# Kernel tuning notes

Measured on AMD Instinct MI355X. Metric: run time of the kernel, lower is better.

Reference implementation:

```python
import jax, jax.numpy as jnp
from jax import lax
import numpy as np

B, L, H, V = 256, 2048, 128, 32000
THR = 0.4      # energy_threshold
LN_EPS = 1e-5  # torch LayerNorm default


def setup_inputs() -> dict:
    key = jax.random.key(0)
    ks = jax.random.split(key, 12)
    s = lambda k, shp, scale: (jax.random.normal(k, shp, dtype=jnp.float32) * scale)
    return {
        "seq": jax.random.randint(ks[0], (B, L), 0, V),
        "embed": s(ks[1], (V, H), 0.02),
        "W1": s(ks[2], (H, 2 * H), H ** -0.5),
        "b1": jnp.zeros((2 * H,), jnp.float32),
        "W2": s(ks[3], (2 * H, H), (2 * H) ** -0.5),
        "b2": jnp.zeros((H,), jnp.float32),
        "gamma": jnp.ones((H,), jnp.float32),
        "beta": jnp.zeros((H,), jnp.float32),
        "Wrp": s(ks[4], (H, H), H ** -0.5),
        "brp": jnp.zeros((H,), jnp.float32),
        "Wout": s(ks[5], (H, V), H ** -0.5),
        "bout": jnp.zeros((V,), jnp.float32),
    }


def _encode(seq, embed, W1, b1, W2, b2, gamma, beta):
    e = embed[seq]                                         # [B,L,H]
    ff = jnp.maximum(e @ W1 + b1, 0.0) @ W2 + b2           # [B,L,H]
    y = e + ff
    mu = y.mean(-1, keepdims=True)
    var = ((y - mu) ** 2).mean(-1, keepdims=True)
    return (y - mu) * lax.rsqrt(var + LN_EPS) * gamma + beta


def reference(seq, embed, W1, b1, W2, b2, gamma, beta, Wrp, brp, Wout, bout):
    h_all = _encode(seq, embed, W1, b1, W2, b2, gamma, beta)  # [B,L,H]

    def step(M, k):
        # k = v = h_all[:, t, :]  -> [B,H]
        v = k
        vp = jnp.einsum('bij,bj->bi', M, k)
        error = v - vp / (jnp.sum(k * k, axis=-1, keepdims=True) + 1e-6)
        gate = (jnp.linalg.norm(error, axis=-1)
                > THR * jnp.linalg.norm(v, axis=-1)).astype(M.dtype)  # [B]
        M = M + gate[:, None, None] * jnp.einsum('bi,bj->bij', error, k)
        return M, None

    M0 = jnp.zeros((B, H, H), h_all.dtype)
    ks = jnp.swapaxes(h_all[:, :-1, :], 0, 1)               # [L-1,B,H]
    M_fin, _ = lax.scan(step, M0, ks)
    r = jnp.einsum('bij,bj->bi', M_fin, h_all[:, -1, :])    # [B,H]
    return (r @ Wrp + brp) @ Wout + bout                    # [B,V]
```

## Files before the change

### kernel.cpp

```cpp
#include <hip/hip_runtime.h>
#include <hip/hip_bf16.h>


#define BB 256
#define LL 2048
#define HH 128
#define VV 32000
#define RS 136

typedef float f32x2 __attribute__((ext_vector_type(2)));

__device__ __forceinline__ void dma16(const float* g, float* l) {
  __builtin_amdgcn_global_load_lds(
      (const __attribute__((address_space(1))) void*)g,
      (__attribute__((address_space(3))) void*)l,
      16, 0, 0);
}

template <int CTRL>
__device__ __forceinline__ float dppadd(float x) {
  int y = __builtin_amdgcn_update_dpp(0, __float_as_int(x), CTRL, 0xF, 0xF, true);
  return x + __int_as_float(y);
}

__device__ __forceinline__ void pkfma(f32x2& d, f32x2 a, f32x2 b) {
  asm("v_pk_fma_f32 %0, %1, %2, %0" : "+v"(d) : "v"(a), "v"(b));
}

__device__ __forceinline__ void barrier_lgkm() {
  asm volatile("s_waitcnt lgkmcnt(0)\n\ts_barrier" ::: "memory");
}
__device__ __forceinline__ void wait_vmN(int n) {
  if (n == 3)      asm volatile("s_waitcnt vmcnt(3)" ::: "memory");
  else if (n == 2) asm volatile("s_waitcnt vmcnt(2)" ::: "memory");
  else if (n == 1) asm volatile("s_waitcnt vmcnt(1)" ::: "memory");
  else             asm volatile("s_waitcnt vmcnt(0)" ::: "memory");
}

__global__ __launch_bounds__(256, 1) void build_htab_kernel(
    const float* __restrict__ embed,
    const float* __restrict__ W1,
    const float* __restrict__ b1,
    const float* __restrict__ W2,
    const float* __restrict__ b2,
    const float* __restrict__ gamma,
    const float* __restrict__ beta,
    float* __restrict__ Htab2)
{
  const int tid = threadIdx.x;
  const int j   = tid & 127;
  const int h2  = tid >> 7;

  float w1r[128];
#pragma unroll
  for (int m = 0; m < 128; ++m) w1r[m] = W1[m * 256 + tid];

  const float b1n = b1[tid];
  const float b2j = b2[j];
  const float gj  = gamma[j];
  const float bj  = beta[j];

  __shared__ __align__(16) float4 w2q[64][128];
  __shared__ __align__(16) float e_s[128];
  __shared__ __align__(16) float a_s[256];
  __shared__ float p_s[2][128];
  __shared__ float red[8];

  for (int idx = tid; idx < 8192; idx += 256) {
    int n4 = idx >> 7, jj = idx & 127;
    float4 w;
    w.x = W2[(size_t)(4 * n4 + 0) * 128 + jj];
    w.y = W2[(size_t)(4 * n4 + 1) * 128 + jj];
    w.z = W2[(size_t)(4 * n4 + 2) * 128 + jj];
    w.w = W2[(size_t)(4 * n4 + 3) * 128 + jj];
    w2q[n4][jj] = w;
  }
  __syncthreads();

  for (int v = blockIdx.x; v < VV; v += gridDim.x) {
    if (tid < 128) e_s[tid] = embed[(size_t)v * 128 + tid];
    __syncthreads();

    float acc[4] = {b1n, 0.f, 0.f, 0.f};
#pragma unroll
    for (int q = 0; q < 32; ++q) {
      float4 ev = *(const float4*)&e_s[4 * q];
      float t = ev.x * w1r[4 * q + 0];
      t = fmaf(ev.y, w1r[4 * q + 1], t);
      t = fmaf(ev.z, w1r[4 * q + 2], t);
      t = fmaf(ev.w, w1r[4 * q + 3], t);
      acc[q & 3] += t;
    }
    float a = fmaxf((acc[0] + acc[1]) + (acc[2] + acc[3]), 0.0f);
    a_s[tid] = a;
    __syncthreads();

    float p0 = 0.f, p1 = 0.f, p2v = 0.f, p3 = 0.f;
#pragma unroll
    for (int q = 0; q < 32; ++q) {
      int n4 = h2 * 32 + q;
      float4 av = *(const float4*)&a_s[4 * n4];
      float4 wq = w2q[n4][j];
      p0 = fmaf(av.x, wq.x, p0);
      p1 = fmaf(av.y, wq.y, p1);
      p2v = fmaf(av.z, wq.z, p2v);
      p3 = fmaf(av.w, wq.w, p3);
    }
    p_s[h2][j] = (p0 + p1) + (p2v + p3);
    __syncthreads();

    float y = 0.0f;
    if (tid < 128) {
      float ff = p_s[0][tid] + p_s[1][tid] + b2j;
      y = e_s[tid] + ff;
    }
    float s1 = y, s2 = y * y;
    s1 = dppadd<0xB1>(s1);  s2 = dppadd<0xB1>(s2);
    s1 = dppadd<0x4E>(s1);  s2 = dppadd<0x4E>(s2);
    s1 = dppadd<0x141>(s1); s2 = dppadd<0x141>(s2);
    s1 = dppadd<0x140>(s1); s2 = dppadd<0x140>(s2);
    s1 = dppadd<0x142>(s1); s2 = dppadd<0x142>(s2);
    s1 = dppadd<0x143>(s1); s2 = dppadd<0x143>(s2);
    if (tid < 128 && (tid & 63) == 63) {
      red[tid >> 6] = s1;
      red[2 + (tid >> 6)] = s2;
    }
    __syncthreads();
    float mu = (red[0] + red[1]) * (1.0f / 128.0f);
    float ms = (red[2] + red[3]) * (1.0f / 128.0f);
    float var = ms - mu * mu;
    float hv = 0.0f;
    if (tid < 128) {
      float dy = y - mu;
      hv = dy * (1.0f / sqrtf(var + 1e-5f)) * gj + bj;
      int ofs = tid + ((tid >> 6) << 2);
      Htab2[(size_t)v * RS + ofs] = hv;
    }
    float q2 = hv * hv;
    q2 = dppadd<0xB1>(q2);
    q2 = dppadd<0x4E>(q2);
    q2 = dppadd<0x141>(q2);
    q2 = dppadd<0x140>(q2);
    q2 = dppadd<0x142>(q2);
    q2 = dppadd<0x143>(q2);
    if (tid < 128 && (tid & 63) == 63) red[4 + (tid >> 6)] = q2;
    __syncthreads();
    if (tid == 0) {
      float kk = red[4] + red[5];
      Htab2[(size_t)v * RS + 132] = kk;
      Htab2[(size_t)v * RS + 133] = 1.0f / (kk + 1e-6f);
    }
    __syncthreads();
  }
}

__global__ __launch_bounds__(512, 1) void scan_kernel(
    const int* __restrict__ seq,
    const float* __restrict__ Htab2,
    const float* __restrict__ Wrp,
    const float* __restrict__ brp,
    float* __restrict__ rr)
{
  const int b     = blockIdx.x;
  const int tid   = threadIdx.x;
  const int lane  = tid & 63;
  const int wv    = tid >> 6;
  const int rg    = lane >> 4;
  const int cg    = lane & 15;
  const int i0    = wv * 16 + rg * 4;
  const int iofs  = i0 + ((i0 >> 6) << 2);
  const int kbase = (cg & 7) * 8 + (cg >> 3) * 68;

  __shared__ int seq_s[LL];
  __shared__ __align__(16) float slots[8][RS];
  __shared__ __align__(16) float red_s[4][8];
  __shared__ __align__(16) float r_s[128];
  __shared__ float p2_s[4][128];

  {
    int t0 = seq[(size_t)b * LL + 0];
    int t1 = seq[(size_t)b * LL + 1];
    int t2 = seq[(size_t)b * LL + 2];
    int t3 = seq[(size_t)b * LL + 3];
    if (lane < 34) {
      dma16(Htab2 + (size_t)t0 * RS + lane * 4, &slots[0][0]);
      dma16(Htab2 + (size_t)t1 * RS + lane * 4, &slots[1][0]);
      dma16(Htab2 + (size_t)t2 * RS + lane * 4, &slots[2][0]);
      dma16(Htab2 + (size_t)t3 * RS + lane * 4, &slots[3][0]);
    }
  }
  for (int t = tid; t < LL; t += 512) seq_s[t] = seq[(size_t)b * LL + t];
  __syncthreads();

  f32x2 M00{0.f,0.f}, M01{0.f,0.f}, M02{0.f,0.f}, M03{0.f,0.f};
  f32x2 M10{0.f,0.f}, M11{0.f,0.f}, M12{0.f,0.f}, M13{0.f,0.f};
  f32x2 M20{0.f,0.f}, M21{0.f,0.f}, M22{0.f,0.f}, M23{0.f,0.f};
  f32x2 M30{0.f,0.f}, M31{0.f,0.f}, M32{0.f,0.f}, M33{0.f,0.f};

  f32x2 kA0, kA1, kA2, kA3, kB0, kB1, kB2, kB3;
  float4 kiA, kiB;
  float kkA, invA, kkB, invB;
  {
    const f32x2* kp = (const f32x2*)&slots[0][kbase];
    kA0 = kp[0]; kA1 = kp[1]; kA2 = kp[2]; kA3 = kp[3];
    kiA = *(const float4*)&slots[0][iofs];
    float2 kv = *(const float2*)&slots[0][132];
    kkA = kv.x; invA = kv.y;
    asm volatile("" : "+v"(kA0), "+v"(kA1), "+v"(kA2), "+v"(kA3));
    asm volatile("" : "+v"(kiA.x), "+v"(kiA.y), "+v"(kiA.z), "+v"(kiA.w));
    asm volatile("" : "+v"(kkA), "+v"(invA));
  }

  auto step = [&](f32x2& kc0, f32x2& kc1, f32x2& kc2, f32x2& kc3,
                  float4& kic, float kk_c, float inv_c,
                  f32x2& kn0, f32x2& kn1, f32x2& kn2, f32x2& kn3,
                  float4& kin, float& kk_n, float& inv_n,
                  int t, int p, int sn, int sd, int nwait) {
    if (nwait == 3) {
      int tk = seq_s[t + 4];
      if (lane < 34)
        dma16(Htab2 + (size_t)tk * RS + lane * 4, &slots[sd][0]);
    }
    f32x2 a0{0.f,0.f}, a1{0.f,0.f}, a2{0.f,0.f}, a3{0.f,0.f};
    pkfma(a0, kc0, M00); pkfma(a0, kc1, M01); pkfma(a0, kc2, M02); pkfma(a0, kc3, M03);
    pkfma(a1, kc0, M10); pkfma(a1, kc1, M11); pkfma(a1, kc2, M12); pkfma(a1, kc3, M13);
    pkfma(a2, kc0, M20); pkfma(a2, kc1, M21); pkfma(a2, kc2, M22); pkfma(a2, kc3, M23);
    pkfma(a3, kc0, M30); pkfma(a3, kc1, M31); pkfma(a3, kc2, M32); pkfma(a3, kc3, M33);
    float v0 = a0.x + a0.y, v1 = a1.x + a1.y;
    float v2 = a2.x + a2.y, v3 = a3.x + a3.y;
    v0 = dppadd<0xB1>(v0);  v1 = dppadd<0xB1>(v1);
    v2 = dppadd<0xB1>(v2);  v3 = dppadd<0xB1>(v3);
    v0 = dppadd<0x4E>(v0);  v1 = dppadd<0x4E>(v1);
    v2 = dppadd<0x4E>(v2);  v3 = dppadd<0x4E>(v3);
    v0 = dppadd<0x141>(v0); v1 = dppadd<0x141>(v1);
    v2 = dppadd<0x141>(v2); v3 = dppadd<0x141>(v3);
    v0 = dppadd<0x140>(v0); v1 = dppadd<0x140>(v1);
    v2 = dppadd<0x140>(v2); v3 = dppadd<0x140>(v3);
    float e0 = fmaf(-v0, inv_c, kic.x);
    float e1 = fmaf(-v1, inv_c, kic.y);
    float e2 = fmaf(-v2, inv_c, kic.z);
    float e3 = fmaf(-v3, inv_c, kic.w);
    float s = fmaf(e3, e3, fmaf(e2, e2, fmaf(e1, e1, e0 * e0)));
    s = dppadd<0x142>(s);
    s = dppadd<0x143>(s);
    if (lane == 63) red_s[p][wv] = s;
    barrier_lgkm();

    float4 ra = *(const float4*)&red_s[p][0];
    float4 rb = *(const float4*)&red_s[p][4];
    wait_vmN(nwait);
    {
      const f32x2* kp = (const f32x2*)&slots[sn][kbase];
      kn0 = kp[0]; kn1 = kp[1]; kn2 = kp[2]; kn3 = kp[3];
      kin = *(const float4*)&slots[sn][iofs];
      float2 kv = *(const float2*)&slots[sn][132];
      kk_n = kv.x; inv_n = kv.y;
    }
    float ne2 = ((ra.x + ra.y) + (ra.z + ra.w)) + ((rb.x + rb.y) + (rb.z + rb.w));
    int g = ne2 > 0.16f * kk_c;
    float ge0 = g ? e0 : 0.0f;
    float ge1 = g ? e1 : 0.0f;
    float ge2 = g ? e2 : 0.0f;
    float ge3 = g ? e3 : 0.0f;
    f32x2 g0{ge0, ge0}, g1{ge1, ge1}, g2{ge2, ge2}, g3{ge3, ge3};
    pkfma(M00, g0, kc0); pkfma(M01, g0, kc1); pkfma(M02, g0, kc2); pkfma(M03, g0, kc3);
    pkfma(M10, g1, kc0); pkfma(M11, g1, kc1); pkfma(M12, g1, kc2); pkfma(M13, g1, kc3);
    pkfma(M20, g2, kc0); pkfma(M21, g2, kc1); pkfma(M22, g2, kc2); pkfma(M23, g2, kc3);
    pkfma(M30, g3, kc0); pkfma(M31, g3, kc1); pkfma(M32, g3, kc2); pkfma(M33, g3, kc3);
    asm volatile("" : "+v"(kn0), "+v"(kn1), "+v"(kn2), "+v"(kn3));
    asm volatile("" : "+v"(kin.x), "+v"(kin.y), "+v"(kin.z), "+v"(kin.w));
    asm volatile("" : "+v"(kk_n), "+v"(inv_n));
  };

  for (int t = 0; t < 2040; t += 8) {
    step(kA0,kA1,kA2,kA3, kiA, kkA, invA, kB0,kB1,kB2,kB3, kiB, kkB, invB, t + 0, 0, 1, 4, 3);
    step(kB0,kB1,kB2,kB3, kiB, kkB, invB, kA0,kA1,kA2,kA3, kiA, kkA, invA, t + 1, 1, 2, 5, 3);
    step(kA0,kA1,kA2,kA3, kiA, kkA, invA, kB0,kB1,kB2,kB3, kiB, kkB, invB, t + 2, 2, 3, 6, 3);
    step(kB0,kB1,kB2,kB3, kiB, kkB, invB, kA0,kA1,kA2,kA3, kiA, kkA, invA, t + 3, 3, 4, 7, 3);
    step(kA0,kA1,kA2,kA3, kiA, kkA, invA, kB0,kB1,kB2,kB3, kiB, kkB, invB, t + 4, 0, 5, 0, 3);
    step(kB0,kB1,kB2,kB3, kiB, kkB, invB, kA0,kA1,kA2,kA3, kiA, kkA, invA, t + 5, 1, 6, 1, 3);
    step(kA0,kA1,kA2,kA3, kiA, kkA, invA, kB0,kB1,kB2,kB3, kiB, kkB, invB, t + 6, 2, 7, 2, 3);
    step(kB0,kB1,kB2,kB3, kiB, kkB, invB, kA0,kA1,kA2,kA3, kiA, kkA, invA, t + 7, 3, 0, 3, 3);
  }
  step(kA0,kA1,kA2,kA3, kiA, kkA, invA, kB0,kB1,kB2,kB3, kiB, kkB, invB, 2040, 0, 1, 4, 3);
  step(kB0,kB1,kB2,kB3, kiB, kkB, invB, kA0,kA1,kA2,kA3, kiA, kkA, invA, 2041, 1, 2, 5, 3);
  step(kA0,kA1,kA2,kA3, kiA, kkA, invA, kB0,kB1,kB2,kB3, kiB, kkB, invB, 2042, 2, 3, 6, 3);
  step(kB0,kB1,kB2,kB3, kiB, kkB, invB, kA0,kA1,kA2,kA3, kiA, kkA, invA, 2043, 3, 4, 7, 3);
  step(kA0,kA1,kA2,kA3, kiA, kkA, invA, kB0,kB1,kB2,kB3, kiB, kkB, invB, 2044, 0, 5, 0, 2);
  step(kB0,kB1,kB2,kB3, kiB, kkB, invB, kA0,kA1,kA2,kA3, kiA, kkA, invA, 2045, 1, 6, 1, 1);
  step(kA0,kA1,kA2,kA3, kiA, kkA, invA, kB0,kB1,kB2,kB3, kiB, kkB, invB, 2046, 2, 7, 2, 0);

  {
    f32x2 a0{0.f,0.f}, a1{0.f,0.f}, a2{0.f,0.f}, a3{0.f,0.f};
    pkfma(a0, kB0, M00); pkfma(a0, kB1, M01); pkfma(a0, kB2, M02); pkfma(a0, kB3, M03);
    pkfma(a1, kB0, M10); pkfma(a1, kB1, M11); pkfma(a1, kB2, M12); pkfma(a1, kB3, M13);
    pkfma(a2, kB0, M20); pkfma(a2, kB1, M21); pkfma(a2, kB2, M22); pkfma(a2, kB3, M23);
    pkfma(a3, kB0, M30); pkfma(a3, kB1, M31); pkfma(a3, kB2, M32); pkfma(a3, kB3, M33);
    float v0 = a0.x + a0.y, v1 = a1.x + a1.y;
    float v2 = a2.x + a2.y, v3 = a3.x + a3.y;
    v0 = dppadd<0xB1>(v0);  v1 = dppadd<0xB1>(v1);
    v2 = dppadd<0xB1>(v2);  v3 = dppadd<0xB1>(v3);
    v0 = dppadd<0x4E>(v0);  v1 = dppadd<0x4E>(v1);
    v2 = dppadd<0x4E>(v2);  v3 = dppadd<0x4E>(v3);
    v0 = dppadd<0x141>(v0); v1 = dppadd<0x141>(v1);
    v2 = dppadd<0x141>(v2); v3 = dppadd<0x141>(v3);
    v0 = dppadd<0x140>(v0); v1 = dppadd<0x140>(v1);
    v2 = dppadd<0x140>(v2); v3 = dppadd<0x140>(v3);
    if (cg == 0) {
      *(float4*)&r_s[i0] = float4{v0, v1, v2, v3};
    }
  }
  __syncthreads();

  const int j = tid & 127;
  const int g = tid >> 7;
  float pac[2] = {0.f, 0.f};
#pragma unroll
  for (int m = 0; m < 32; ++m) {
    pac[m & 1] = fmaf(r_s[g * 32 + m],
                      Wrp[(size_t)(g * 32 + m) * 128 + j], pac[m & 1]);
  }
  p2_s[g][j] = pac[0] + pac[1];
  __syncthreads();
  if (tid < 128) {
    rr[(size_t)b * 128 + tid] =
        p2_s[0][tid] + p2_s[1][tid] + p2_s[2][tid] + p2_s[3][tid] + brp[tid];
  }
}

__global__ __launch_bounds__(256, 1) void out_kernel(
    const float* __restrict__ rr,
    const float* __restrict__ Wout,
    const float* __restrict__ bout,
    float* __restrict__ out)
{
  const int tid = threadIdx.x;
  const int v = blockIdx.x * 64 + (tid & 63);
  const int bg = tid >> 6;
  const int b0 = blockIdx.y * 64;

  __shared__ float4 rs4[64][32];
  for (int idx = tid; idx < 2048; idx += 256) {
    int bb = idx >> 5, q = idx & 31;
    rs4[bb][q] = ((const float4*)rr)[(size_t)(b0 + bb) * 32 + q];
  }
  __syncthreads();

  float acc[16];
#pragma unroll
  for (int m = 0; m < 16; ++m) acc[m] = 0.0f;

  for (int h4 = 0; h4 < 32; ++h4) {
    float w0 = Wout[(size_t)(4 * h4 + 0) * VV + v];
    float w1 = Wout[(size_t)(4 * h4 + 1) * VV + v];
    float w2 = Wout[(size_t)(4 * h4 + 2) * VV + v];
    float w3 = Wout[(size_t)(4 * h4 + 3) * VV + v];
#pragma unroll
    for (int m = 0; m < 16; ++m) {
      float4 rv = rs4[bg * 16 + m][h4];
      float t = rv.x * w0;
      t = fmaf(rv.y, w1, t);
      t = fmaf(rv.z, w2, t);
      t = fmaf(rv.w, w3, t);
      acc[m] += t;
    }
  }
  float bo = bout[v];
#pragma unroll
  for (int m = 0; m < 16; ++m) {
    out[(size_t)(b0 + bg * 16 + m) * VV + v] = acc[m] + bo;
  }
}

extern "C" void kernel_launch(void* const* d_in, const int* in_sizes, int n_in,
                              void* d_out, int out_size, void* d_ws, size_t ws_size,
                              hipStream_t stream)
{
  const int* seq      = (const int*)d_in[0];
  const float* embed  = (const float*)d_in[1];
  const float* W1     = (const float*)d_in[2];
  const float* b1     = (const float*)d_in[3];
  const float* W2     = (const float*)d_in[4];
  const float* b2     = (const float*)d_in[5];
  const float* gamma  = (const float*)d_in[6];
  const float* beta   = (const float*)d_in[7];
  const float* Wrp    = (const float*)d_in[8];
  const float* brp    = (const float*)d_in[9];
  const float* Wout   = (const float*)d_in[10];
  const float* bout   = (const float*)d_in[11];
  float* out          = (float*)d_out;

  char* ws = (char*)d_ws;
  float* Htab2 = (float*)ws;
  float* rr    = (float*)(ws + 17408000);

  hipLaunchKernelGGL(build_htab_kernel, dim3(256), dim3(256), 0, stream,
                     embed, W1, b1, W2, b2, gamma, beta, Htab2);
  hipLaunchKernelGGL(scan_kernel, dim3(BB), dim3(512), 0, stream,
                     seq, Htab2, Wrp, brp, rr);
  hipLaunchKernelGGL(out_kernel, dim3(VV / 64, 4), dim3(256), 0, stream,
                     rr, Wout, bout, out);
}
```

Baseline: 1.460 ms.

## Process two scan steps per barrier using rank-one correction algebra

Restructures the sequential delta-rule scan so each block handles two tokens per superstep. The second token's error and gate are derived algebraically from the first token's error (via e·a, e·e, k0·k1 dot products reduced together), so only one cross-wave barrier and reduction is needed per two steps. This halves the barrier and LDS reduction count on the serial critical path, at the cost of extra FMAs, more registers for two in-flight token sets, and reordered floating-point arithmetic that may differ slightly near the gate threshold.

```diff
diff --git a/kernel.cpp b/kernel.cpp
--- a/kernel.cpp
+++ b/kernel.cpp
@@ -31,8 +31,7 @@
   asm volatile("s_waitcnt lgkmcnt(0)\n\ts_barrier" ::: "memory");
 }
 __device__ __forceinline__ void wait_vmN(int n) {
-  if (n == 3)      asm volatile("s_waitcnt vmcnt(3)" ::: "memory");
-  else if (n == 2) asm volatile("s_waitcnt vmcnt(2)" ::: "memory");
+  if (n == 2)      asm volatile("s_waitcnt vmcnt(2)" ::: "memory");
   else if (n == 1) asm volatile("s_waitcnt vmcnt(1)" ::: "memory");
   else             asm volatile("s_waitcnt vmcnt(0)" ::: "memory");
 }
@@ -173,9 +172,16 @@
 
   __shared__ int seq_s[LL];
   __shared__ __align__(16) float slots[8][RS];
-  __shared__ __align__(16) float red_s[4][8];
+  __shared__ __align__(16) float4 red4[3][8];
+  __shared__ __align__(16) float red1[8];
   __shared__ __align__(16) float r_s[128];
   __shared__ float p2_s[4][128];
+
+  struct KTok {
+    f32x2 c0, c1, c2, c3;
+    float ki0, ki1, ki2, ki3;
+    float kk, inv;
+  };
 
   {
     int t0 = seq[(size_t)b * LL + 0];
@@ -197,37 +203,26 @@
   f32x2 M20{0.f,0.f}, M21{0.f,0.f}, M22{0.f,0.f}, M23{0.f,0.f};
   f32x2 M30{0.f,0.f}, M31{0.f,0.f}, M32{0.f,0.f}, M33{0.f,0.f};
 
-  f32x2 kA0, kA1, kA2, kA3, kB0, kB1, kB2, kB3;
-  float4 kiA, kiB;
-  float kkA, invA, kkB, invB;
-  {
-    const f32x2* kp = (const f32x2*)&slots[0][kbase];
-    kA0 = kp[0]; kA1 = kp[1]; kA2 = kp[2]; kA3 = kp[3];
-    kiA = *(const float4*)&slots[0][iofs];
-    float2 kv = *(const float2*)&slots[0][132];
-    kkA = kv.x; invA = kv.y;
-    asm volatile("" : "+v"(kA0), "+v"(kA1), "+v"(kA2), "+v"(kA3));
-    asm volatile("" : "+v"(kiA.x), "+v"(kiA.y), "+v"(kiA.z), "+v"(kiA.w));
-    asm volatile("" : "+v"(kkA), "+v"(invA));
-  }
-
-  auto step = [&](f32x2& kc0, f32x2& kc1, f32x2& kc2, f32x2& kc3,
-                  float4& kic, float kk_c, float inv_c,
-                  f32x2& kn0, f32x2& kn1, f32x2& kn2, f32x2& kn3,
-                  float4& kin, float& kk_n, float& inv_n,
-                  int t, int p, int sn, int sd, int nwait) {
-    if (nwait == 3) {
-      int tk = seq_s[t + 4];
-      if (lane < 34)
-        dma16(Htab2 + (size_t)tk * RS + lane * 4, &slots[sd][0]);
-    }
+  auto loadTok = [&](KTok& T, const float* sp) {
+    const f32x2* kp = (const f32x2*)(sp + kbase);
+    T.c0 = kp[0]; T.c1 = kp[1]; T.c2 = kp[2]; T.c3 = kp[3];
+    float4 k4 = *(const float4*)(sp + iofs);
+    T.ki0 = k4.x; T.ki1 = k4.y; T.ki2 = k4.z; T.ki3 = k4.w;
+    float2 kv = *(const float2*)(sp + 132);
+    T.kk = kv.x; T.inv = kv.y;
+  };
+  auto pinTok = [&](KTok& T) {
+    asm volatile("" : "+v"(T.c0), "+v"(T.c1), "+v"(T.c2), "+v"(T.c3));
+    asm volatile("" : "+v"(T.ki0), "+v"(T.ki1), "+v"(T.ki2), "+v"(T.ki3));
+    asm volatile("" : "+v"(T.kk), "+v"(T.inv));
+  };
+  auto rowdot = [&](const KTok& K, float& v0, float& v1, float& v2, float& v3) {
     f32x2 a0{0.f,0.f}, a1{0.f,0.f}, a2{0.f,0.f}, a3{0.f,0.f};
-    pkfma(a0, kc0, M00); pkfma(a0, kc1, M01); pkfma(a0, kc2, M02); pkfma(a0, kc3, M03);
-    pkfma(a1, kc0, M10); pkfma(a1, kc1, M11); pkfma(a1, kc2, M12); pkfma(a1, kc3, M13);
-    pkfma(a2, kc0, M20); pkfma(a2, kc1, M21); pkfma(a2, kc2, M22); pkfma(a2, kc3, M23);
-    pkfma(a3, kc0, M30); pkfma(a3, kc1, M31); pkfma(a3, kc2, M32); pkfma(a3, kc3, M33);
-    float v0 = a0.x + a0.y, v1 = a1.x + a1.y;
-    float v2 = a2.x + a2.y, v3 = a3.x + a3.y;
+    pkfma(a0, K.c0, M00); pkfma(a0, K.c1, M01); pkfma(a0, K.c2, M02); pkfma(a0, K.c3, M03);
+    pkfma(a1, K.c0, M10); pkfma(a1, K.c1, M11); pkfma(a1, K.c2, M12); pkfma(a1, K.c3, M13);
+    pkfma(a2, K.c0, M20); pkfma(a2, K.c1, M21); pkfma(a2, K.c2, M22); pkfma(a2, K.c3, M23);
+    pkfma(a3, K.c0, M30); pkfma(a3, K.c1, M31); pkfma(a3, K.c2, M32); pkfma(a3, K.c3, M33);
+    v0 = a0.x + a0.y; v1 = a1.x + a1.y; v2 = a2.x + a2.y; v3 = a3.x + a3.y;
     v0 = dppadd<0xB1>(v0);  v1 = dppadd<0xB1>(v1);
     v2 = dppadd<0xB1>(v2);  v3 = dppadd<0xB1>(v3);
     v0 = dppadd<0x4E>(v0);  v1 = dppadd<0x4E>(v1);
@@ -236,76 +231,125 @@
     v2 = dppadd<0x141>(v2); v3 = dppadd<0x141>(v3);
     v0 = dppadd<0x140>(v0); v1 = dppadd<0x140>(v1);
     v2 = dppadd<0x140>(v2); v3 = dppadd<0x140>(v3);
-    float e0 = fmaf(-v0, inv_c, kic.x);
-    float e1 = fmaf(-v1, inv_c, kic.y);
-    float e2 = fmaf(-v2, inv_c, kic.z);
-    float e3 = fmaf(-v3, inv_c, kic.w);
+  };
+
+  KTok P0{}, P1{}, Q0{}, Q1{};
+  loadTok(P0, &slots[0][0]);
+  loadTok(P1, &slots[1][0]);
+  pinTok(P0); pinTok(P1);
+
+  int p = 0;
+
+  auto superstep = [&](KTok& C0, KTok& C1, KTok& R0, KTok& R1,
+                       int t, int sr0, int sr1, int sd0, int sd1,
+                       int nwait, int doIssue) {
+    if (doIssue) {
+      int tk0 = seq_s[t + 4];
+      int tk1 = seq_s[t + 5];
+      if (lane < 34) {
+        dma16(Htab2 + (size_t)tk0 * RS + lane * 4, &slots[sd0][0]);
+        dma16(Htab2 + (size_t)tk1 * RS + lane * 4, &slots[sd1][0]);
+      }
+    }
+    float u0, u1, u2, u3, w0, w1, w2, w3;
+    rowdot(C0, u0, u1, u2, u3);
+    rowdot(C1, w0, w1, w2, w3);
+    float e0 = fmaf(-C0.inv, u0, C0.ki0);
+    float e1 = fmaf(-C0.inv, u1, C0.ki1);
+    float e2 = fmaf(-C0.inv, u2, C0.ki2);
+    float e3 = fmaf(-C0.inv, u3, C0.ki3);
+    float aa0 = fmaf(-C1.inv, w0, C1.ki0);
+    float aa1 = fmaf(-C1.inv, w1, C1.ki1);
+    float aa2 = fmaf(-C1.inv, w2, C1.ki2);
+    float aa3 = fmaf(-C1.inv, w3, C1.ki3);
+    float sE  = fmaf(e3, e3, fmaf(e2, e2, fmaf(e1, e1, e0 * e0)));
+    float sC  = fmaf(C0.ki3, C1.ki3, fmaf(C0.ki2, C1.ki2, fmaf(C0.ki1, C1.ki1, C0.ki0 * C1.ki0)));
+    float sAE = fmaf(aa3, e3, fmaf(aa2, e2, fmaf(aa1, e1, aa0 * e0)));
+    float sA  = fmaf(aa3, aa3, fmaf(aa2, aa2, fmaf(aa1, aa1, aa0 * aa0)));
+    sE = dppadd<0x142>(sE);  sC = dppadd<0x142>(sC);
+    sAE = dppadd<0x142>(sAE); sA = dppadd<0x142>(sA);
+    sE = dppadd<0x143>(sE);  sC = dppadd<0x143>(sC);
+    sAE = dppadd<0x143>(sAE); sA = dppadd<0x143>(sA);
+    if (lane == 63) red4[p][wv] = float4{sE, sC, sAE, sA};
+    barrier_lgkm();
+    const float4* rp = (const float4*)&red4[p][0];
+    float4 q0 = rp[0], q1 = rp[1], q2 = rp[2], q3 = rp[3];
+    float4 q4 = rp[4], q5 = rp[5], q6 = rp[6], q7 = rp[7];
+    wait_vmN(nwait);
+    loadTok(R0, &slots[sr0][0]);
+    loadTok(R1, &slots[sr1][0]);
+    float SE  = ((q0.x + q1.x) + (q2.x + q3.x)) + ((q4.x + q5.x) + (q6.x + q7.x));
+    float SC  = ((q0.y + q1.y) + (q2.y + q3.y)) + ((q4.y + q5.y) + (q6.y + q7.y));
+    float SAE = ((q0.z + q1.z) + (q2.z + q3.z)) + ((q4.z + q5.z) + (q6.z + q7.z));
+    float SA  = ((q0.w + q1.w) + (q2.w + q3.w)) + ((q4.w + q5.w) + (q6.w + q7.w));
+    int gA = SE > 0.16f * C0.kk;
+    float phi = gA ? (C1.inv * SC) : 0.0f;
+    float E1 = fmaf(phi, fmaf(phi, SE, -2.0f * SAE), SA);
+    int gB = E1 > 0.16f * C1.kk;
+    float f0 = gA ? e0 : 0.0f;
+    float f1 = gA ? e1 : 0.0f;
+    float f2 = gA ? e2 : 0.0f;
+    float f3 = gA ? e3 : 0.0f;
+    float h0 = fmaf(-phi, e0, aa0);
+    float h1 = fmaf(-phi, e1, aa1);
+    float h2 = fmaf(-phi, e2, aa2);
+    float h3 = fmaf(-phi, e3, aa3);
+    float j0 = gB ? h0 : 0.0f;
+    float j1 = gB ? h1 : 0.0f;
+    float j2 = gB ? h2 : 0.0f;
+    float j3 = gB ? h3 : 0.0f;
+    f32x2 F0{f0, f0}, F1{f1, f1}, F2{f2, f2}, F3{f3, f3};
+    f32x2 J0{j0, j0}, J1{j1, j1}, J2{j2, j2}, J3{j3, j3};
+    pkfma(M00, F0, C0.c0); pkfma(M01, F0, C0.c1); pkfma(M02, F0, C0.c2); pkfma(M03, F0, C0.c3);
+    pkfma(M10, F1, C0.c0); pkfma(M11, F1, C0.c1); pkfma(M12, F1, C0.c2); pkfma(M13, F1, C0.c3);
+    pkfma(M20, F2, C0.c0); pkfma(M21, F2, C0.c1); pkfma(M22, F2, C0.c2); pkfma(M23, F2, C0.c3);
+    pkfma(M30, F3, C0.c0); pkfma(M31, F3, C0.c1); pkfma(M32, F3, C0.c2); pkfma(M33, F3, C0.c3);
+    pkfma(M00, J0, C1.c0); pkfma(M01, J0, C1.c1); pkfma(M02, J0, C1.c2); pkfma(M03, J0, C1.c3);
+    pkfma(M10, J1, C1.c0); pkfma(M11, J1, C1.c1); pkfma(M12, J1, C1.c2); pkfma(M13, J1, C1.c3);
+    pkfma(M20, J2, C1.c0); pkfma(M21, J2, C1.c1); pkfma(M22, J2, C1.c2); pkfma(M23, J2, C1.c3);
+    pkfma(M30, J3, C1.c0); pkfma(M31, J3, C1.c1); pkfma(M32, J3, C1.c2); pkfma(M33, J3, C1.c3);
+    pinTok(R0); pinTok(R1);
+    p = (p == 2) ? 0 : (p + 1);
+  };
+
+  for (int it = 0; it < 255; ++it) {
+    int T = it * 8;
+    superstep(P0, P1, Q0, Q1, T + 0, 2, 3, 4, 5, 2, 1);
+    superstep(Q0, Q1, P0, P1, T + 2, 4, 5, 6, 7, 2, 1);
+    superstep(P0, P1, Q0, Q1, T + 4, 6, 7, 0, 1, 2, 1);
+    superstep(Q0, Q1, P0, P1, T + 6, 0, 1, 2, 3, 2, 1);
+  }
+  superstep(P0, P1, Q0, Q1, 2040, 2, 3, 4, 5, 2, 1);
+  superstep(Q0, Q1, P0, P1, 2042, 4, 5, 6, 7, 2, 1);
+  superstep(P0, P1, Q0, Q1, 2044, 6, 7, 0, 1, 0, 0);
+
+  {
+    float u0, u1, u2, u3;
+    rowdot(Q0, u0, u1, u2, u3);
+    float e0 = fmaf(-Q0.inv, u0, Q0.ki0);
+    float e1 = fmaf(-Q0.inv, u1, Q0.ki1);
+    float e2 = fmaf(-Q0.inv, u2, Q0.ki2);
+    float e3 = fmaf(-Q0.inv, u3, Q0.ki3);
     float s = fmaf(e3, e3, fmaf(e2, e2, fmaf(e1, e1, e0 * e0)));
     s = dppadd<0x142>(s);
     s = dppadd<0x143>(s);
-    if (lane == 63) red_s[p][wv] = s;
+    if (lane == 63) red1[wv] = s;
     barrier_lgkm();
-
-    float4 ra = *(const float4*)&red_s[p][0];
-    float4 rb = *(const float4*)&red_s[p][4];
-    wait_vmN(nwait);
-    {
-      const f32x2* kp = (const f32x2*)&slots[sn][kbase];
-      kn0 = kp[0]; kn1 = kp[1]; kn2 = kp[2]; kn3 = kp[3];
-      kin = *(const float4*)&slots[sn][iofs];
-      float2 kv = *(const float2*)&slots[sn][132];
-      kk_n = kv.x; inv_n = kv.y;
-    }
-    float ne2 = ((ra.x + ra.y) + (ra.z + ra.w)) + ((rb.x + rb.y) + (rb.z + rb.w));
-    int g = ne2 > 0.16f * kk_c;
-    float ge0 = g ? e0 : 0.0f;
-    float ge1 = g ? e1 : 0.0f;
-    float ge2 = g ? e2 : 0.0f;
-    float ge3 = g ? e3 : 0.0f;
-    f32x2 g0{ge0, ge0}, g1{ge1, ge1}, g2{ge2, ge2}, g3{ge3, ge3};
-    pkfma(M00, g0, kc0); pkfma(M01, g0, kc1); pkfma(M02, g0, kc2); pkfma(M03, g0, kc3);
-    pkfma(M10, g1, kc0); pkfma(M11, g1, kc1); pkfma(M12, g1, kc2); pkfma(M13, g1, kc3);
-    pkfma(M20, g2, kc0); pkfma(M21, g2, kc1); pkfma(M22, g2, kc2); pkfma(M23, g2, kc3);
-    pkfma(M30, g3, kc0); pkfma(M31, g3, kc1); pkfma(M32, g3, kc2); pkfma(M33, g3, kc3);
-    asm volatile("" : "+v"(kn0), "+v"(kn1), "+v"(kn2), "+v"(kn3));
-    asm volatile("" : "+v"(kin.x), "+v"(kin.y), "+v"(kin.z), "+v"(kin.w));
-    asm volatile("" : "+v"(kk_n), "+v"(inv_n));
-  };
-
-  for (int t = 0; t < 2040; t += 8) {
-    step(kA0,kA1,kA2,kA3, kiA, kkA, invA, kB0,kB1,kB2,kB3, kiB, kkB, invB, t + 0, 0, 1, 4, 3);
-    step(kB0,kB1,kB2,kB3, kiB, kkB, invB, kA0,kA1,kA2,kA3, kiA, kkA, invA, t + 1, 1, 2, 5, 3);
-    step(kA0,kA1,kA2,kA3, kiA, kkA, invA, kB0,kB1,kB2,kB3, kiB, kkB, invB, t + 2, 2, 3, 6, 3);
-    step(kB0,kB1,kB2,kB3, kiB, kkB, invB, kA0,kA1,kA2,kA3, kiA, kkA, invA, t + 3, 3, 4, 7, 3);
-    step(kA0,kA1,kA2,kA3, kiA, kkA, invA, kB0,kB1,kB2,kB3, kiB, kkB, invB, t + 4, 0, 5, 0, 3);
-    step(kB0,kB1,kB2,kB3, kiB, kkB, invB, kA0,kA1,kA2,kA3, kiA, kkA, invA, t + 5, 1, 6, 1, 3);
-    step(kA0,kA1,kA2,kA3, kiA, kkA, invA, kB0,kB1,kB2,kB3, kiB, kkB, invB, t + 6, 2, 7, 2, 3);
-    step(kB0,kB1,kB2,kB3, kiB, kkB, invB, kA0,kA1,kA2,kA3, kiA, kkA, invA, t + 7, 3, 0, 3, 3);
-  }
-  step(kA0,kA1,kA2,kA3, kiA, kkA, invA, kB0,kB1,kB2,kB3, kiB, kkB, invB, 2040, 0, 1, 4, 3);
-  step(kB0,kB1,kB2,kB3, kiB, kkB, invB, kA0,kA1,kA2,kA3, kiA, kkA, invA, 2041, 1, 2, 5, 3);
-  step(kA0,kA1,kA2,kA3, kiA, kkA, invA, kB0,kB1,kB2,kB3, kiB, kkB, invB, 2042, 2, 3, 6, 3);
-  step(kB0,kB1,kB2,kB3, kiB, kkB, invB, kA0,kA1,kA2,kA3, kiA, kkA, invA, 2043, 3, 4, 7, 3);
-  step(kA0,kA1,kA2,kA3, kiA, kkA, invA, kB0,kB1,kB2,kB3, kiB, kkB, invB, 2044, 0, 5, 0, 2);
-  step(kB0,kB1,kB2,kB3, kiB, kkB, invB, kA0,kA1,kA2,kA3, kiA, kkA, invA, 2045, 1, 6, 1, 1);
-  step(kA0,kA1,kA2,kA3, kiA, kkA, invA, kB0,kB1,kB2,kB3, kiB, kkB, invB, 2046, 2, 7, 2, 0);
-
-  {
-    f32x2 a0{0.f,0.f}, a1{0.f,0.f}, a2{0.f,0.f}, a3{0.f,0.f};
-    pkfma(a0, kB0, M00); pkfma(a0, kB1, M01); pkfma(a0, kB2, M02); pkfma(a0, kB3, M03);
-    pkfma(a1, kB0, M10); pkfma(a1, kB1, M11); pkfma(a1, kB2, M12); pkfma(a1, kB3, M13);
-    pkfma(a2, kB0, M20); pkfma(a2, kB1, M21); pkfma(a2, kB2, M22); pkfma(a2, kB3, M23);
-    pkfma(a3, kB0, M30); pkfma(a3, kB1, M31); pkfma(a3, kB2, M32); pkfma(a3, kB3, M33);
-    float v0 = a0.x + a0.y, v1 = a1.x + a1.y;
-    float v2 = a2.x + a2.y, v3 = a3.x + a3.y;
-    v0 = dppadd<0xB1>(v0);  v1 = dppadd<0xB1>(v1);
-    v2 = dppadd<0xB1>(v2);  v3 = dppadd<0xB1>(v3);
-    v0 = dppadd<0x4E>(v0);  v1 = dppadd<0x4E>(v1);
-    v2 = dppadd<0x4E>(v2);  v3 = dppadd<0x4E>(v3);
-    v0 = dppadd<0x141>(v0); v1 = dppadd<0x141>(v1);
-    v2 = dppadd<0x141>(v2); v3 = dppadd<0x141>(v3);
-    v0 = dppadd<0x140>(v0); v1 = dppadd<0x140>(v1);
-    v2 = dppadd<0x140>(v2); v3 = dppadd<0x140>(v3);
+    float4 ra = *(const float4*)&red1[0];
+    float4 rb = *(const float4*)&red1[4];
+    float SE = ((ra.x + ra.y) + (ra.z + ra.w)) + ((rb.x + rb.y) + (rb.z + rb.w));
+    int g = SE > 0.16f * Q0.kk;
+    float f0 = g ? e0 : 0.0f;
+    float f1 = g ? e1 : 0.0f;
+    float f2 = g ? e2 : 0.0f;
+    float f3 = g ? e3 : 0.0f;
+    f32x2 F0{f0, f0}, F1{f1, f1}, F2{f2, f2}, F3{f3, f3};
+    pkfma(M00, F0, Q0.c0); pkfma(M01, F0, Q0.c1); pkfma(M02, F0, Q0.c2); pkfma(M03, F0, Q0.c3);
+    pkfma(M10, F1, Q0.c0); pkfma(M11, F1, Q0.c1); pkfma(M12, F1, Q0.c2); pkfma(M13, F1, Q0.c3);
+    pkfma(M20, F2, Q0.c0); pkfma(M21, F2, Q0.c1); pkfma(M22, F2, Q0.c2); pkfma(M23, F2, Q0.c3);
+    pkfma(M30, F3, Q0.c0); pkfma(M31, F3, Q0.c1); pkfma(M32, F3, Q0.c2); pkfma(M33, F3, Q0.c3);
+    float v0, v1, v2, v3;
+    rowdot(Q1, v0, v1, v2, v3);
     if (cg == 0) {
       *(float4*)&r_s[i0] = float4{v0, v1, v2, v3};
     }
```

Result: slower. 1.620 ms (+10.9%).
